# Performance work log

Measured on AMD Instinct MI355X. Metric: run time of the kernel, lower is better.

## Reference

```python
import jax, jax.numpy as jnp
import numpy as np

N_USERS = 100000
N_ITEMS = 50000
N_NODES = N_USERS + N_ITEMS
EMB_DIM = 64
N_EDGES = 1200000
N_LAYERS = 3


def setup_inputs() -> dict:
    key = jax.random.key(0)
    k1, k2, k3, k4, k5 = jax.random.split(key, 5)
    edge_row = jax.random.randint(k1, (N_EDGES,), 0, N_NODES, dtype=jnp.int32)
    edge_col = jax.random.randint(k2, (N_EDGES,), 0, N_NODES, dtype=jnp.int32)
    edge_weight = jax.random.uniform(k3, (N_EDGES,), dtype=jnp.float32)
    # xavier_uniform for nn.Embedding: bound = sqrt(6/(fan_in+fan_out))
    bu = float(np.sqrt(6.0 / (N_USERS + EMB_DIM)))
    bi = float(np.sqrt(6.0 / (N_ITEMS + EMB_DIM)))
    user_emb = jax.random.uniform(k4, (N_USERS, EMB_DIM), jnp.float32, -bu, bu)
    item_emb = jax.random.uniform(k5, (N_ITEMS, EMB_DIM), jnp.float32, -bi, bi)
    return {
        "edge_row": edge_row,
        "edge_col": edge_col,
        "edge_weight": edge_weight,
        "user_emb": user_emb,
        "item_emb": item_emb,
    }


def _spmm(edge_row, edge_col, edge_weight, x):
    # y[i] = sum_{e: row[e]==i} w[e] * x[col[e]]  (COO sparse @ dense)
    gathered = x[edge_col] * edge_weight[:, None]  # [E, d]
    return jax.ops.segment_sum(gathered, edge_row, num_segments=N_NODES)


def reference(edge_row, edge_col, edge_weight, user_emb, item_emb):
    x = jnp.concatenate([user_emb, item_emb], axis=0)  # [N, d]
    acc = x  # running sum over layer outputs (layer 0 = initial embeddings)
    for _ in range(N_LAYERS):
        x = _spmm(edge_row, edge_col, edge_weight, x)
        acc = acc + x
    mean_emb = acc / (N_LAYERS + 1)
    return mean_emb[:N_USERS], mean_emb[N_USERS:]
```

## Files before the change

kernel.cpp:

```cpp
#include <hip/hip_runtime.h>
#include <hip/hip_bf16.h>


#define EMB 64
#define BUCKET_SHIFT 7
#define BROWS (1 << BUCKET_SHIFT)
#define LROW 65
#define NBUCK_PAD 1184
#define S1_CHUNK 2048
#define BCAP 1408
#define ACC_SCALE 1048576.0f
#define ACC_INV (1.0f / 1048576.0f)

typedef _Float16 h8 __attribute__((ext_vector_type(8)));
typedef float f4 __attribute__((ext_vector_type(4)));

union H8U { h8 v; _Float16 e[8]; };

__global__ void s1_convert(const int* __restrict__ row, const int* __restrict__ col,
                           const float* __restrict__ w, int* __restrict__ cursor1,
                           int2* __restrict__ tmp,
                           const float* __restrict__ ue, const float* __restrict__ ie,
                           h8* __restrict__ X0h, int nu_elems, int total8,
                           int E, int s1Blocks) {
    int t = threadIdx.x;
    if ((int)blockIdx.x < s1Blocks) {
        __shared__ int lcount[NBUCK_PAD];
        __shared__ int lbase[NBUCK_PAD];
        int c0 = blockIdx.x * S1_CHUNK;
        for (int i = t; i < NBUCK_PAD; i += 512) lcount[i] = 0;
        __syncthreads();
        int pkc[S1_CHUNK / 512];
        int cc[S1_CHUNK / 512];
        int rr[S1_CHUNK / 512];
        float ww[S1_CHUNK / 512];
        #pragma unroll
        for (int i = 0; i < S1_CHUNK / 512; i++) {
            int e = c0 + i * 512 + t;
            pkc[i] = -1;
            if (e < E) {
                int r = row[e];
                int b = r >> BUCKET_SHIFT;
                int rank = atomicAdd(&lcount[b], 1);
                pkc[i] = (b << 12) | rank;
                cc[i] = col[e];
                rr[i] = r & (BROWS - 1);
                ww[i] = w[e];
            }
        }
        __syncthreads();
        for (int i = t; i < NBUCK_PAD; i += 512) {
            int c = lcount[i];
            if (c) lbase[i] = atomicAdd(&cursor1[i], c);
        }
        __syncthreads();
        #pragma unroll
        for (int i = 0; i < S1_CHUNK / 512; i++) {
            if (pkc[i] >= 0) {
                int b = pkc[i] >> 12;
                int pos = lbase[b] + (pkc[i] & 4095);
                if (pos < BCAP)
                    tmp[(size_t)b * BCAP + pos] =
                        make_int2((cc[i] << BUCKET_SHIFT) | rr[i], __float_as_int(ww[i]));
            }
        }
    } else {
        int g = (blockIdx.x - s1Blocks) * 512 + t;
        if (g >= total8) return;
        int base = g << 3;
        const f4* src = (const f4*)((base < nu_elems) ? (ue + base)
                                                      : (ie + (base - nu_elems)));
        f4 a = src[0], b = src[1];
        h8 o;
        o[0] = (_Float16)a.x; o[1] = (_Float16)a.y; o[2] = (_Float16)a.z; o[3] = (_Float16)a.w;
        o[4] = (_Float16)b.x; o[5] = (_Float16)b.y; o[6] = (_Float16)b.z; o[7] = (_Float16)b.w;
        X0h[g] = o;
    }
}

template <bool LAST>
__global__ __launch_bounds__(512) void spmm_bucket(
        const int* __restrict__ cursor1, const int2* __restrict__ tmp,
        const h8* __restrict__ Xin, h8* __restrict__ Xout,
        const h8* __restrict__ X0, const h8* __restrict__ X1,
        float* __restrict__ out, int nrows) {
    __shared__ int acc[BROWS * LROW];
    int t = threadIdx.x;
    int b = blockIdx.x;

    int4* az = (int4*)acc;
    for (int i = t; i < BROWS * LROW / 4; i += 512) az[i] = make_int4(0, 0, 0, 0);
    __syncthreads();

    int num = cursor1[b];
    if (num > BCAP) num = BCAP;
    const int2* ebase = tmp + (size_t)b * BCAP;

    int g = t >> 3;
    int l8 = t & 7;

    int e = g;
    for (; e + 64 < num; e += 128) {
        int2 r0 = ebase[e];
        int2 r1 = ebase[e + 64];
        H8U v0, v1;
        v0.v = Xin[((r0.x >> BUCKET_SHIFT) << 3) + l8];
        v1.v = Xin[((r1.x >> BUCKET_SHIFT) << 3) + l8];
        float w0 = __int_as_float(r0.y) * ACC_SCALE;
        float w1 = __int_as_float(r1.y) * ACC_SCALE;
        int* d0 = &acc[(r0.x & (BROWS - 1)) * LROW + l8 * 8];
        int* d1 = &acc[(r1.x & (BROWS - 1)) * LROW + l8 * 8];
        #pragma unroll
        for (int k = 0; k < 8; k++) atomicAdd(&d0[k], __float2int_rn(w0 * (float)v0.e[k]));
        #pragma unroll
        for (int k = 0; k < 8; k++) atomicAdd(&d1[k], __float2int_rn(w1 * (float)v1.e[k]));
    }
    for (; e < num; e += 64) {
        int2 r0 = ebase[e];
        H8U v0;
        v0.v = Xin[((r0.x >> BUCKET_SHIFT) << 3) + l8];
        float w0 = __int_as_float(r0.y) * ACC_SCALE;
        int* d0 = &acc[(r0.x & (BROWS - 1)) * LROW + l8 * 8];
        #pragma unroll
        for (int k = 0; k < 8; k++) atomicAdd(&d0[k], __float2int_rn(w0 * (float)v0.e[k]));
    }
    __syncthreads();

    int rowbase = b << BUCKET_SHIFT;
    int rows_here = nrows - rowbase;
    if (rows_here > BROWS) rows_here = BROWS;
    for (int i = t; i < rows_here * 8; i += 512) {
        int r = i >> 3, c8 = i & 7;
        int rowid = rowbase + r;
        const int* src = &acc[r * LROW + c8 * 8];
        if (LAST) {
            h8 x0 = X0[(rowid << 3) + c8];
            h8 v1 = X1[(rowid << 3) + c8];
            h8 v2 = Xin[(rowid << 3) + c8];
            int base = (rowid << 6) + (c8 << 3);
            f4 o0, o1;
            o0.x = 0.25f * ((float)x0[0] + (float)v1[0] + (float)v2[0] + (float)src[0] * ACC_INV);
            o0.y = 0.25f * ((float)x0[1] + (float)v1[1] + (float)v2[1] + (float)src[1] * ACC_INV);
            o0.z = 0.25f * ((float)x0[2] + (float)v1[2] + (float)v2[2] + (float)src[2] * ACC_INV);
            o0.w = 0.25f * ((float)x0[3] + (float)v1[3] + (float)v2[3] + (float)src[3] * ACC_INV);
            o1.x = 0.25f * ((float)x0[4] + (float)v1[4] + (float)v2[4] + (float)src[4] * ACC_INV);
            o1.y = 0.25f * ((float)x0[5] + (float)v1[5] + (float)v2[5] + (float)src[5] * ACC_INV);
            o1.z = 0.25f * ((float)x0[6] + (float)v1[6] + (float)v2[6] + (float)src[6] * ACC_INV);
            o1.w = 0.25f * ((float)x0[7] + (float)v1[7] + (float)v2[7] + (float)src[7] * ACC_INV);
            f4* dst = (f4*)(out + base);
            dst[0] = o0;
            dst[1] = o1;
        } else {
            h8 o;
            #pragma unroll
            for (int k = 0; k < 8; k++) o[k] = (_Float16)((float)src[k] * ACC_INV);
            Xout[(rowid << 3) + c8] = o;
        }
    }
}

extern "C" void kernel_launch(void* const* d_in, const int* in_sizes, int n_in,
                              void* d_out, int out_size, void* d_ws, size_t ws_size,
                              hipStream_t stream) {
    const int* edge_row = (const int*)d_in[0];
    const int* edge_col = (const int*)d_in[1];
    const float* edge_w = (const float*)d_in[2];
    const float* user_emb = (const float*)d_in[3];
    const float* item_emb = (const float*)d_in[4];

    const int E = in_sizes[0];
    const int nu_elems = in_sizes[3];
    const int ni_elems = in_sizes[4];
    const int total = nu_elems + ni_elems;
    const int N = total / EMB;
    const int NBUCK = (N + BROWS - 1) >> BUCKET_SHIFT;

    size_t off = 0;
    auto carve = [&](size_t bytes) {
        void* p = (char*)d_ws + off;
        off += (bytes + 255) & ~(size_t)255;
        return p;
    };
    h8*    X0h     = (h8*)carve((size_t)total * 2);
    h8*    X1h     = (h8*)carve((size_t)total * 2);
    h8*    X2h     = (h8*)carve((size_t)total * 2);
    int*   cursor1 = (int*)carve((size_t)NBUCK * 4);
    int2*  tmp     = (int2*)carve((size_t)NBUCK * BCAP * 8);
    (void)ws_size;

    float* out = (float*)d_out;

    const int total8 = total / 8;
    const int s1Blocks = (E + S1_CHUNK - 1) / S1_CHUNK;
    const int convBlocks = (total8 + 511) / 512;

    hipMemsetAsync(cursor1, 0, (size_t)NBUCK * 4, stream);
    s1_convert<<<s1Blocks + convBlocks, 512, 0, stream>>>(
        edge_row, edge_col, edge_w, cursor1, tmp,
        user_emb, item_emb, X0h, nu_elems, total8, E, s1Blocks);

    spmm_bucket<false><<<NBUCK, 512, 0, stream>>>(cursor1, tmp,
                                                  X0h, X1h, nullptr, nullptr,
                                                  nullptr, N);
    spmm_bucket<false><<<NBUCK, 512, 0, stream>>>(cursor1, tmp,
                                                  X1h, X2h, nullptr, nullptr,
                                                  nullptr, N);
    spmm_bucket<true><<<NBUCK, 512, 0, stream>>>(cursor1, tmp,
                                                 X2h, nullptr, X0h, X1h,
                                                 out, N);
}
```

Measured before the change: 218.3 us.

## Stage bucketed edges in shared memory before coalesced scatter to global

The edge bucketing pass now computes a block-wide exclusive scan of per-bucket counts, writes edges into a shared-memory staging buffer sorted by bucket, then writes them out so consecutive threads store consecutive slots within each bucket. This replaces fully random 8-byte global scatter stores with runs of contiguous writes per bucket. It costs extra shared memory (about 30KB more per block), which may lower occupancy, plus an additional scan and two extra barriers.

```diff
diff --git a/kernel.cpp b/kernel.cpp
--- a/kernel.cpp
+++ b/kernel.cpp
@@ -27,7 +27,13 @@
     if ((int)blockIdx.x < s1Blocks) {
         __shared__ int lcount[NBUCK_PAD];
         __shared__ int lbase[NBUCK_PAD];
+        __shared__ int lexcl[NBUCK_PAD];
+        __shared__ int2 staged[S1_CHUNK];
+        __shared__ short sbkt[S1_CHUNK];
+        __shared__ int swS[8];
         int c0 = blockIdx.x * S1_CHUNK;
+        int chunk_valid = E - c0;
+        if (chunk_valid > S1_CHUNK) chunk_valid = S1_CHUNK;
         for (int i = t; i < NBUCK_PAD; i += 512) lcount[i] = 0;
         __syncthreads();
         int pkc[S1_CHUNK / 512];
@@ -49,20 +55,48 @@
             }
         }
         __syncthreads();
-        for (int i = t; i < NBUCK_PAD; i += 512) {
-            int c = lcount[i];
-            if (c) lbase[i] = atomicAdd(&cursor1[i], c);
+        int lane = t & 63, wave = t >> 6;
+        int b0 = t * 3;
+        int c0v = (b0     < NBUCK_PAD) ? lcount[b0]     : 0;
+        int c1v = (b0 + 1 < NBUCK_PAD) ? lcount[b0 + 1] : 0;
+        int c2v = (b0 + 2 < NBUCK_PAD) ? lcount[b0 + 2] : 0;
+        if (b0     < NBUCK_PAD && c0v) lbase[b0]     = atomicAdd(&cursor1[b0],     c0v);
+        if (b0 + 1 < NBUCK_PAD && c1v) lbase[b0 + 1] = atomicAdd(&cursor1[b0 + 1], c1v);
+        if (b0 + 2 < NBUCK_PAD && c2v) lbase[b0 + 2] = atomicAdd(&cursor1[b0 + 2], c2v);
+        int tsum = c0v + c1v + c2v;
+        int s = tsum;
+        #pragma unroll
+        for (int off = 1; off < 64; off <<= 1) {
+            int tt = __shfl_up(s, off, 64);
+            if (lane >= off) s += tt;
+        }
+        if (lane == 63) swS[wave] = s;
+        __syncthreads();
+        {
+            int woff = 0;
+            for (int wv_ = 0; wv_ < wave; wv_++) woff += swS[wv_];
+            int texcl = woff + s - tsum;
+            if (b0     < NBUCK_PAD) lexcl[b0]     = texcl;
+            if (b0 + 1 < NBUCK_PAD) lexcl[b0 + 1] = texcl + c0v;
+            if (b0 + 2 < NBUCK_PAD) lexcl[b0 + 2] = texcl + c0v + c1v;
         }
         __syncthreads();
         #pragma unroll
         for (int i = 0; i < S1_CHUNK / 512; i++) {
             if (pkc[i] >= 0) {
                 int b = pkc[i] >> 12;
-                int pos = lbase[b] + (pkc[i] & 4095);
-                if (pos < BCAP)
-                    tmp[(size_t)b * BCAP + pos] =
-                        make_int2((cc[i] << BUCKET_SHIFT) | rr[i], __float_as_int(ww[i]));
+                int si = lexcl[b] + (pkc[i] & 4095);
+                staged[si] = make_int2((cc[i] << BUCKET_SHIFT) | rr[i],
+                                       __float_as_int(ww[i]));
+                sbkt[si] = (short)b;
             }
+        }
+        __syncthreads();
+        for (int i = t; i < chunk_valid; i += 512) {
+            int b = sbkt[i];
+            int pos = lbase[b] + (i - lexcl[b]);
+            if (pos < BCAP)
+                tmp[(size_t)b * BCAP + pos] = staged[i];
         }
     } else {
         int g = (blockIdx.x - s1Blocks) * 512 + t;
```

Result: slower. 229.5 us (+5.1%).
